# Performance work log

Measured on AMD Instinct MI355X. Metric: run time of the kernel, lower is better.

The kernel has to match this reference:

```python
import jax, jax.numpy as jnp
import numpy as np

L = 6          # n_layers
D = 128        # patch_dim
COND = 128     # cond_dim
HID = 256      # hidden (fixed default in AffineCoupling)
DIN = D // 2 + COND  # 192, input dim of coupling net


def setup_inputs() -> dict:
    key = jax.random.key(0)
    ks = jax.random.split(key, 8)
    x = jax.random.normal(ks[0], (512, 128, D), dtype=jnp.float32)
    cond = jax.random.normal(ks[1], (512, COND), dtype=jnp.float32)
    # per-layer weights stacked over L; stored [in, out] (torch Linear transposed)
    W1 = jax.random.normal(ks[2], (L, DIN, HID), dtype=jnp.float32) * 0.05
    b1 = jnp.zeros((L, HID), dtype=jnp.float32)
    W2 = jax.random.normal(ks[3], (L, HID, HID), dtype=jnp.float32) * 0.05
    b2 = jnp.zeros((L, HID), dtype=jnp.float32)
    W3 = jax.random.normal(ks[4], (L, HID, D), dtype=jnp.float32) * 0.05
    b3 = jnp.zeros((L, D), dtype=jnp.float32)
    return {"x": x, "cond": cond, "W1": W1, "b1": b1, "W2": W2, "b2": b2, "W3": W3, "b3": b3}


def reference(x, cond, W1, b1, W2, b2, W3, b3):
    B, P, Dd = x.shape
    # cond is shared across patches: broadcast to [B, P, COND]
    condb = jnp.broadcast_to(cond[:, None, :], (B, P, cond.shape[-1]))
    z = x
    logdet = jnp.zeros((B,), dtype=x.dtype)
    for i in range(W1.shape[0]):
        x1, x2 = jnp.split(z, 2, axis=-1)                       # [B,P,D/2] each
        h = jnp.concatenate([x1, condb], axis=-1)               # [B,P,DIN]
        h = jax.nn.relu(jnp.einsum('bpi,ih->bph', h, W1[i]) + b1[i])
        h = jax.nn.relu(jnp.einsum('bph,hk->bpk', h, W2[i]) + b2[i])
        st = jnp.einsum('bpk,kd->bpd', h, W3[i]) + b3[i]        # [B,P,D]
        s, t = jnp.split(st, 2, axis=-1)
        s = jnp.tanh(s) * 0.5
        y2 = x2 * jnp.exp(s) + t
        z = jnp.concatenate([x1, y2], axis=-1)[..., ::-1]        # flip feature dim
        logdet = logdet + s.sum(axis=(1, 2))
    return z, logdet
```

## Files before the change

### kernel.cpp

```cpp
#include <hip/hip_runtime.h>
#include <stdint.h>

#define NLAYERS 6
#define DD      128
#define CONDD   128
#define HID     256
#define DIN     192
#define TM      64
#define NTHR    512
#define SA      72
#define SB      264

typedef __attribute__((ext_vector_type(4))) float f32x4;
typedef __attribute__((ext_vector_type(8))) short short8;

#define G1_KS 2
#define G2_KS 8
#define G3_KS 8
#define G1_FR (G1_KS*16)
#define G2_FR (G2_KS*16)
#define G3_FR (G3_KS*8)
#define FR_L  (G1_FR+G2_FR+G3_FR)
#define EL_L  (FR_L*512)
#define G2_OFF (G1_FR*512)
#define G3_OFF ((G1_FR+G2_FR)*512)

__device__ __forceinline__ short f2bf(float f) {
  uint32_t u = __builtin_bit_cast(uint32_t, f);
  u += 0x7fffu + ((u >> 16) & 1u);
  return (short)(u >> 16);
}
__device__ __forceinline__ uint32_t cvtpk(float lo, float hi) {
  uint32_t r;
  asm("v_cvt_pk_bf16_f32 %0, %1, %2" : "=v"(r) : "v"(lo), "v"(hi));
  return r;
}
__device__ __forceinline__ int kinv(int p) {
  return (p & ~63) | (p & 32) | ((p & 1) << 4) | ((p >> 1) & 15);
}

__global__ void prep_weights(const float* __restrict__ W1,
                             const float* __restrict__ W2,
                             const float* __restrict__ W3,
                             short* __restrict__ wp)
{
  int t = blockIdx.x * 256 + threadIdx.x;
  int lay  = t / (FR_L * 64);
  int rem  = t - lay * (FR_L * 64);
  int frag = rem >> 6;
  int lane = rem & 63;
  const float* src;
  int N, f2, dstbase, nfr, perm;
  if (frag < G1_FR) {
    f2 = frag;                  src = W1 + (size_t)lay * DIN * HID; N = HID; dstbase = 0;      nfr = 16; perm = 0;
  } else if (frag < G1_FR + G2_FR) {
    f2 = frag - G1_FR;          src = W2 + (size_t)lay * HID * HID; N = HID; dstbase = G2_OFF; nfr = 16; perm = 1;
  } else {
    f2 = frag - (G1_FR + G2_FR);src = W3 + (size_t)lay * HID * DD;  N = DD;  dstbase = G3_OFF; nfr = 8;  perm = 2;
  }
  int ks = f2 / nfr, nf = f2 - ks * nfr;
  int lv = lane & 15;
  int n;
  if (perm == 2) {
    int g = nf >> 1, h = nf & 1;
    int c = 16 * g + lv;
    if (lay & 1) c = 63 - c;
    n = c + 64 * h;
  } else {
    n = nf * 16 + lv;
  }
  int k0 = ks * 32 + (lane >> 4) * 8;
  short8 v;
#pragma unroll
  for (int j = 0; j < 8; ++j) {
    int k = perm ? kinv(k0 + j) : (k0 + j);
    v[j] = f2bf(src[(size_t)k * N + n]);
  }
  *(short8*)(wp + (size_t)lay * EL_L + dstbase + ((size_t)f2 * 64 + lane) * 8) = v;
}

__global__ void prep_c1(const float* __restrict__ cond, const float* __restrict__ W1,
                        const float* __restrict__ b1, float* __restrict__ c1)
{
  int lay = blockIdx.x >> 9;
  int b   = blockIdx.x & 511;
  int h   = threadIdx.x;
  const float* wb = W1 + (size_t)lay * DIN * HID + 64 * HID + h;
  const float* cb = cond + b * CONDD;
  float acc = b1[lay * HID + h];
#pragma unroll 4
  for (int c = 0; c < CONDD; ++c) acc = fmaf(cb[c], wb[(size_t)c * HID], acc);
  c1[((size_t)lay * 512 + b) * HID + h] = acc;
}

__global__ __launch_bounds__(NTHR, 4)
void flow_kernel(const float* __restrict__ x,
                 const float* __restrict__ c1g, const float* __restrict__ b2g,
                 const float* __restrict__ b3g, const short* __restrict__ wp,
                 float* __restrict__ outz, float* __restrict__ outld)
{
  __shared__ alignas(16) short bufA[TM * SA];
  __shared__ alignas(16) short bufB[TM * SB];
  __shared__ alignas(16) short bufC[TM * SB];
  __shared__ float red[8];

  const int tid  = threadIdx.x;
  const int wave = tid >> 6;
  const int lane = tid & 63;
  const int l15  = lane & 15;
  const int l4   = lane >> 4;
  const int mh   = wave >> 2;
  const int nq   = wave & 3;
  const int t0   = blockIdx.x * TM;
  const int batch = t0 >> 7;

  const int cB = 16 * nq + l15;
  const int rbase = 32 * mh + 4 * l4;
  float zlo[8], zhi[8];
  {
    const float* xb = x + (size_t)t0 * DD;
#pragma unroll
    for (int m2 = 0; m2 < 2; ++m2)
#pragma unroll
      for (int r = 0; r < 4; ++r) {
        int j = m2 * 4 + r;
        int row = rbase + 16 * m2 + r;
        zlo[j] = xb[row * DD + cB];
        zhi[j] = xb[row * DD + 64 + cB];
      }
#pragma unroll
    for (int m2 = 0; m2 < 2; ++m2)
#pragma unroll
      for (int r = 0; r < 4; ++r) {
        int row = rbase + 16 * m2 + r;
        bufA[row * SA + cB] = f2bf(zlo[m2 * 4 + r]);
      }
  }
  float ldsum = 0.f;
  const f32x4 vzero = {0.f, 0.f, 0.f, 0.f};
  __syncthreads();

#pragma unroll 1
  for (int lay = 0; lay < NLAYERS; ++lay) {
    const short* wl = wp + (size_t)lay * EL_L;
    const int cl = (lay & 1) ? (63 - cB) : cB;

    {
      f32x4 acc[2][4];
#pragma unroll
      for (int m2 = 0; m2 < 2; ++m2)
#pragma unroll
        for (int nf = 0; nf < 4; ++nf) acc[m2][nf] = vzero;
#pragma unroll 1
      for (int ks = 0; ks < G1_KS; ++ks) {
        short8 bb[4];
#pragma unroll
        for (int nf = 0; nf < 4; ++nf)
          bb[nf] = *(const short8*)(wl + (((ks * 16 + 4 * nq + nf) * 64 + lane) * 8));
#pragma unroll
        for (int m2 = 0; m2 < 2; ++m2) {
          int row = 32 * mh + 16 * m2 + l15;
          short8 a = *(const short8*)(bufA + row * SA + ks * 32 + l4 * 8);
#pragma unroll
          for (int nf = 0; nf < 4; ++nf)
            acc[m2][nf] = __builtin_amdgcn_mfma_f32_16x16x32_bf16(a, bb[nf], acc[m2][nf], 0, 0, 0);
        }
      }
      const float* c1row = c1g + ((size_t)lay * 512 + batch) * HID;
#pragma unroll
      for (int h = 0; h < 2; ++h) {
        int c0 = 64 * nq + 32 * h + l15;
        float bias0 = c1row[c0], bias1 = c1row[c0 + 16];
#pragma unroll
        for (int m2 = 0; m2 < 2; ++m2)
#pragma unroll
          for (int r = 0; r < 4; ++r) {
            int row = rbase + 16 * m2 + r;
            float v0 = fmaxf(acc[m2][2 * h][r] + bias0, 0.f);
            float v1 = fmaxf(acc[m2][2 * h + 1][r] + bias1, 0.f);
            *(uint32_t*)(bufB + row * SB + 64 * nq + 32 * h + 2 * l15) = cvtpk(v0, v1);
          }
      }
    }
    __syncthreads();

    {
      const short* wg = wl + G2_OFF;
      f32x4 acc[2][4];
#pragma unroll
      for (int m2 = 0; m2 < 2; ++m2)
#pragma unroll
        for (int nf = 0; nf < 4; ++nf) acc[m2][nf] = vzero;
#pragma unroll 2
      for (int ks = 0; ks < G2_KS; ++ks) {
        short8 bb[4];
#pragma unroll
        for (int nf = 0; nf < 4; ++nf)
          bb[nf] = *(const short8*)(wg + (((ks * 16 + 4 * nq + nf) * 64 + lane) * 8));
#pragma unroll
        for (int m2 = 0; m2 < 2; ++m2) {
          int row = 32 * mh + 16 * m2 + l15;
          short8 a = *(const short8*)(bufB + row * SB + ks * 32 + l4 * 8);
#pragma unroll
          for (int nf = 0; nf < 4; ++nf)
            acc[m2][nf] = __builtin_amdgcn_mfma_f32_16x16x32_bf16(a, bb[nf], acc[m2][nf], 0, 0, 0);
        }
      }
#pragma unroll
      for (int h = 0; h < 2; ++h) {
        int c0 = 64 * nq + 32 * h + l15;
        float bias0 = b2g[lay * HID + c0], bias1 = b2g[lay * HID + c0 + 16];
#pragma unroll
        for (int m2 = 0; m2 < 2; ++m2)
#pragma unroll
          for (int r = 0; r < 4; ++r) {
            int row = rbase + 16 * m2 + r;
            float v0 = fmaxf(acc[m2][2 * h][r] + bias0, 0.f);
            float v1 = fmaxf(acc[m2][2 * h + 1][r] + bias1, 0.f);
            *(uint32_t*)(bufC + row * SB + 64 * nq + 32 * h + 2 * l15) = cvtpk(v0, v1);
          }
      }
    }
    __syncthreads();

    {
      f32x4 acc3[2][2];
#pragma unroll
      for (int m2 = 0; m2 < 2; ++m2) { acc3[m2][0] = vzero; acc3[m2][1] = vzero; }
#pragma unroll 2
      for (int ks = 0; ks < G3_KS; ++ks) {
        short8 bb[2];
#pragma unroll
        for (int nf = 0; nf < 2; ++nf)
          bb[nf] = *(const short8*)(wl + G3_OFF + (((ks * 8 + 2 * nq + nf) * 64 + lane) * 8));
#pragma unroll
        for (int m2 = 0; m2 < 2; ++m2) {
          int row = 32 * mh + 16 * m2 + l15;
          short8 a = *(const short8*)(bufC + row * SB + ks * 32 + l4 * 8);
          acc3[m2][0] = __builtin_amdgcn_mfma_f32_16x16x32_bf16(a, bb[0], acc3[m2][0], 0, 0, 0);
          acc3[m2][1] = __builtin_amdgcn_mfma_f32_16x16x32_bf16(a, bb[1], acc3[m2][1], 0, 0, 0);
        }
      }
      float bias_s = b3g[lay * DD + cl];
      float bias_t = b3g[lay * DD + 64 + cl];
#pragma unroll
      for (int m2 = 0; m2 < 2; ++m2)
#pragma unroll
        for (int r = 0; r < 4; ++r) {
          int j = m2 * 4 + r;
          float sr = acc3[m2][0][r] + bias_s;
          sr = fminf(fmaxf(sr, -8.f), 8.f);
          float tt = acc3[m2][1][r] + bias_t;
          float e2 = __expf(2.f * sr);
          float s  = 0.5f * (e2 - 1.f) / (e2 + 1.f);
          ldsum += s;
          float y2 = fmaf(zhi[j], __expf(s), tt);
          zhi[j] = zlo[j];
          zlo[j] = y2;
        }
      if (lay < NLAYERS - 1) {
        int cn = 63 - cl;
#pragma unroll
        for (int m2 = 0; m2 < 2; ++m2)
#pragma unroll
          for (int r = 0; r < 4; ++r) {
            int row = rbase + 16 * m2 + r;
            bufA[row * SA + cn] = f2bf(zlo[m2 * 4 + r]);
          }
        __syncthreads();
      }
    }
  }

  {
    float* ob = outz + (size_t)t0 * DD;
#pragma unroll
    for (int m2 = 0; m2 < 2; ++m2)
#pragma unroll
      for (int r = 0; r < 4; ++r) {
        int j = m2 * 4 + r;
        int row = rbase + 16 * m2 + r;
        ob[row * DD + cB]      = zlo[j];
        ob[row * DD + 64 + cB] = zhi[j];
      }
  }
#pragma unroll
  for (int off = 32; off > 0; off >>= 1) ldsum += __shfl_down(ldsum, off);
  if (lane == 0) red[wave] = ldsum;
  __syncthreads();
  if (tid == 0) {
    float s = 0.f;
#pragma unroll
    for (int w = 0; w < 8; ++w) s += red[w];
    atomicAdd(&outld[batch], s);
  }
}

extern "C" void kernel_launch(void* const* d_in, const int* in_sizes, int n_in,
                              void* d_out, int out_size, void* d_ws, size_t ws_size,
                              hipStream_t stream)
{
  (void)in_sizes; (void)n_in; (void)out_size; (void)ws_size;
  const float* x   = (const float*)d_in[0];
  const float* cnd = (const float*)d_in[1];
  const float* W1  = (const float*)d_in[2];
  const float* b1  = (const float*)d_in[3];
  const float* W2  = (const float*)d_in[4];
  const float* b2  = (const float*)d_in[5];
  const float* W3  = (const float*)d_in[6];
  const float* b3  = (const float*)d_in[7];
  float* outz  = (float*)d_out;
  float* outld = outz + (size_t)512 * 128 * 128;
  short* wp = (short*)d_ws;
  float* c1 = (float*)((char*)d_ws + (2u << 20));

  hipMemsetAsync(outld, 0, 512 * sizeof(float), stream);
  prep_weights<<<336, 256, 0, stream>>>(W1, W2, W3, wp);
  prep_c1<<<6 * 512, 256, 0, stream>>>(cnd, W1, b1, c1);
  flow_kernel<<<1024, NTHR, 0, stream>>>(x, c1, b2, b3, wp, outz, outld);
}
```

Measured before the change: 160.6 us.

## Drop second LDS activation buffer, fold biases into accumulator init, raise occupancy hint

The GEMM2 output now overwrites bufB in place after an extra barrier, which removes bufC and cuts LDS per block by roughly half. This should let more 512-thread blocks fit per CU, and the launch bound is raised from 4 to 6 to match. Biases are loaded into the MFMA accumulators as their initial values instead of being added in the epilogue. The costs are one extra __syncthreads per layer and a tighter register budget under the higher occupancy target, which could cause spills.

```diff
diff --git a/kernel.cpp b/kernel.cpp
--- a/kernel.cpp
+++ b/kernel.cpp
@@ -93,7 +93,7 @@
   c1[((size_t)lay * 512 + b) * HID + h] = acc;
 }
 
-__global__ __launch_bounds__(NTHR, 4)
+__global__ __launch_bounds__(NTHR, 6)
 void flow_kernel(const float* __restrict__ x,
                  const float* __restrict__ c1g, const float* __restrict__ b2g,
                  const float* __restrict__ b3g, const short* __restrict__ wp,
@@ -101,7 +101,6 @@
 {
   __shared__ alignas(16) short bufA[TM * SA];
   __shared__ alignas(16) short bufB[TM * SB];
-  __shared__ alignas(16) short bufC[TM * SB];
   __shared__ float red[8];
 
   const int tid  = threadIdx.x;
@@ -137,7 +136,6 @@
       }
   }
   float ldsum = 0.f;
-  const f32x4 vzero = {0.f, 0.f, 0.f, 0.f};
   __syncthreads();
 
 #pragma unroll 1
@@ -146,11 +144,14 @@
     const int cl = (lay & 1) ? (63 - cB) : cB;
 
     {
+      const float* c1row = c1g + ((size_t)lay * 512 + batch) * HID;
       f32x4 acc[2][4];
 #pragma unroll
-      for (int m2 = 0; m2 < 2; ++m2)
-#pragma unroll
-        for (int nf = 0; nf < 4; ++nf) acc[m2][nf] = vzero;
+      for (int nf = 0; nf < 4; ++nf) {
+        float b = c1row[64 * nq + 16 * nf + l15];
+        f32x4 bi = {b, b, b, b};
+        acc[0][nf] = bi; acc[1][nf] = bi;
+      }
 #pragma unroll 1
       for (int ks = 0; ks < G1_KS; ++ks) {
         short8 bb[4];
@@ -166,21 +167,17 @@
             acc[m2][nf] = __builtin_amdgcn_mfma_f32_16x16x32_bf16(a, bb[nf], acc[m2][nf], 0, 0, 0);
         }
       }
-      const float* c1row = c1g + ((size_t)lay * 512 + batch) * HID;
-#pragma unroll
-      for (int h = 0; h < 2; ++h) {
-        int c0 = 64 * nq + 32 * h + l15;
-        float bias0 = c1row[c0], bias1 = c1row[c0 + 16];
+#pragma unroll
+      for (int h = 0; h < 2; ++h)
 #pragma unroll
         for (int m2 = 0; m2 < 2; ++m2)
 #pragma unroll
           for (int r = 0; r < 4; ++r) {
             int row = rbase + 16 * m2 + r;
-            float v0 = fmaxf(acc[m2][2 * h][r] + bias0, 0.f);
-            float v1 = fmaxf(acc[m2][2 * h + 1][r] + bias1, 0.f);
+            float v0 = fmaxf(acc[m2][2 * h][r], 0.f);
+            float v1 = fmaxf(acc[m2][2 * h + 1][r], 0.f);
             *(uint32_t*)(bufB + row * SB + 64 * nq + 32 * h + 2 * l15) = cvtpk(v0, v1);
           }
-      }
     }
     __syncthreads();
 
@@ -188,9 +185,11 @@
       const short* wg = wl + G2_OFF;
       f32x4 acc[2][4];
 #pragma unroll
-      for (int m2 = 0; m2 < 2; ++m2)
-#pragma unroll
-        for (int nf = 0; nf < 4; ++nf) acc[m2][nf] = vzero;
+      for (int nf = 0; nf < 4; ++nf) {
+        float b = b2g[lay * HID + 64 * nq + 16 * nf + l15];
+        f32x4 bi = {b, b, b, b};
+        acc[0][nf] = bi; acc[1][nf] = bi;
+      }
 #pragma unroll 2
       for (int ks = 0; ks < G2_KS; ++ks) {
         short8 bb[4];
@@ -206,27 +205,30 @@
             acc[m2][nf] = __builtin_amdgcn_mfma_f32_16x16x32_bf16(a, bb[nf], acc[m2][nf], 0, 0, 0);
         }
       }
-#pragma unroll
-      for (int h = 0; h < 2; ++h) {
-        int c0 = 64 * nq + 32 * h + l15;
-        float bias0 = b2g[lay * HID + c0], bias1 = b2g[lay * HID + c0 + 16];
+      __syncthreads();
+#pragma unroll
+      for (int h = 0; h < 2; ++h)
 #pragma unroll
         for (int m2 = 0; m2 < 2; ++m2)
 #pragma unroll
           for (int r = 0; r < 4; ++r) {
             int row = rbase + 16 * m2 + r;
-            float v0 = fmaxf(acc[m2][2 * h][r] + bias0, 0.f);
-            float v1 = fmaxf(acc[m2][2 * h + 1][r] + bias1, 0.f);
-            *(uint32_t*)(bufC + row * SB + 64 * nq + 32 * h + 2 * l15) = cvtpk(v0, v1);
+            float v0 = fmaxf(acc[m2][2 * h][r], 0.f);
+            float v1 = fmaxf(acc[m2][2 * h + 1][r], 0.f);
+            *(uint32_t*)(bufB + row * SB + 64 * nq + 32 * h + 2 * l15) = cvtpk(v0, v1);
           }
-      }
     }
     __syncthreads();
 
     {
       f32x4 acc3[2][2];
-#pragma unroll
-      for (int m2 = 0; m2 < 2; ++m2) { acc3[m2][0] = vzero; acc3[m2][1] = vzero; }
+      {
+        float bs = b3g[lay * DD + cl];
+        float bt = b3g[lay * DD + 64 + cl];
+        f32x4 bsi = {bs, bs, bs, bs}, bti = {bt, bt, bt, bt};
+        acc3[0][0] = bsi; acc3[1][0] = bsi;
+        acc3[0][1] = bti; acc3[1][1] = bti;
+      }
 #pragma unroll 2
       for (int ks = 0; ks < G3_KS; ++ks) {
         short8 bb[2];
@@ -236,21 +238,18 @@
 #pragma unroll
         for (int m2 = 0; m2 < 2; ++m2) {
           int row = 32 * mh + 16 * m2 + l15;
-          short8 a = *(const short8*)(bufC + row * SB + ks * 32 + l4 * 8);
+          short8 a = *(const short8*)(bufB + row * SB + ks * 32 + l4 * 8);
           acc3[m2][0] = __builtin_amdgcn_mfma_f32_16x16x32_bf16(a, bb[0], acc3[m2][0], 0, 0, 0);
           acc3[m2][1] = __builtin_amdgcn_mfma_f32_16x16x32_bf16(a, bb[1], acc3[m2][1], 0, 0, 0);
         }
       }
-      float bias_s = b3g[lay * DD + cl];
-      float bias_t = b3g[lay * DD + 64 + cl];
 #pragma unroll
       for (int m2 = 0; m2 < 2; ++m2)
 #pragma unroll
         for (int r = 0; r < 4; ++r) {
           int j = m2 * 4 + r;
-          float sr = acc3[m2][0][r] + bias_s;
-          sr = fminf(fmaxf(sr, -8.f), 8.f);
-          float tt = acc3[m2][1][r] + bias_t;
+          float sr = fminf(fmaxf(acc3[m2][0][r], -8.f), 8.f);
+          float tt = acc3[m2][1][r];
           float e2 = __expf(2.f * sr);
           float s  = 0.5f * (e2 - 1.f) / (e2 + 1.f);
           ldsum += s;
```

After: 188.6 us. +17.5%, slower.
